# Kernel tuning notes

Hardware: AMD Instinct MI355X
Metric: run time of the kernel (lower is better)

## Reference

```python
import jax, jax.numpy as jnp
import numpy as np

GROUPS = 3
EPS = 1e-5

def _conv(x, w, groups, pad):
    # x: NCHW, w: OIHW (grouped). pad: 'VALID' for 1x1, ((1,1),(1,1)) for 3x3 same.
    return jax.lax.conv_general_dilated(
        x, w, window_strides=(1, 1), padding=pad,
        feature_group_count=groups,
        dimension_numbers=('NCHW', 'OIHW', 'NCHW'))

def _bn(x, g, b, m, v):
    # folded inference batchnorm: y = x*scale + (beta - mean*scale)
    s = g / jnp.sqrt(v + EPS)
    return x * s[None, :, None, None] + (b - m * s)[None, :, None, None]

def _shuffle(x, groups):
    B, C, H, W = x.shape
    return x.reshape(B, groups, C // groups, H, W).transpose(0, 2, 1, 3, 4).reshape(B, C, H, W)

def setup_inputs() -> dict:
    key = jax.random.key(0)
    ks = jax.random.split(key, 16)
    B, Cin, Cout, H, W = 64, 480, 480, 28, 28
    mid = Cout // 4  # 120
    d = {}
    d['x'] = jax.random.normal(ks[0], (B, Cin, H, W), jnp.float32)
    d['w1'] = jax.random.normal(ks[1], (mid, Cin // GROUPS, 1, 1), jnp.float32) * 0.05
    d['g1'] = jax.random.uniform(ks[2], (mid,), jnp.float32)
    d['b1'] = jax.random.normal(ks[3], (mid,), jnp.float32)
    d['m1'] = jax.random.normal(ks[4], (mid,), jnp.float32)
    d['v1'] = jax.random.uniform(ks[5], (mid,), jnp.float32)
    d['w2'] = jax.random.normal(ks[6], (mid, 1, 3, 3), jnp.float32) * 0.05
    d['g2'] = jax.random.uniform(ks[7], (mid,), jnp.float32)
    d['b2'] = jax.random.normal(ks[8], (mid,), jnp.float32)
    d['m2'] = jax.random.normal(ks[9], (mid,), jnp.float32)
    d['v2'] = jax.random.uniform(ks[10], (mid,), jnp.float32)
    d['w3'] = jax.random.normal(ks[11], (Cout, mid // GROUPS, 1, 1), jnp.float32) * 0.05
    d['g3'] = jax.random.uniform(ks[12], (Cout,), jnp.float32)
    d['b3'] = jax.random.normal(ks[13], (Cout,), jnp.float32)
    d['m3'] = jax.random.normal(ks[14], (Cout,), jnp.float32)
    d['v3'] = jax.random.uniform(ks[15], (Cout,), jnp.float32)
    return d

def reference(x, w1, g1, b1, m1, v1, w2, g2, b2, m2, v2, w3, g3, b3, m3, v3):
    mid = w2.shape[0]
    shortcut = x  # in_channels == out_channels -> identity shortcut
    out = jax.nn.relu(_bn(_conv(x, w1, GROUPS, 'VALID'), g1, b1, m1, v1))
    out = _bn(_conv(out, w2, mid, ((1, 1), (1, 1))), g2, b2, m2, v2)  # depthwise 3x3
    out = _shuffle(out, GROUPS)
    out = jax.nn.relu(_bn(_conv(out, w3, GROUPS, 'VALID'), g3, b3, m3, v3))
    return out + shortcut
```

## Files before the change

### kernel.cpp

```cpp
#include <hip/hip_runtime.h>


namespace {
constexpr int CIN = 480;
constexpr int MID = 120;
constexpr int HWP = 784;
constexpr float EPSV = 1e-5f;

constexpr size_t TMP1_N = (size_t)64 * MID * HWP;
constexpr int WA1_N = 3 * 3 * 5 * 64 * 8;
constexpr int WA3_N = 3 * 10 * 2 * 64 * 8;

constexpr int S1W = 84;
constexpr int S1O = 65;
constexpr int S2O = 69;
constexpr int S3O = 67;
}

typedef short bf16x8 __attribute__((ext_vector_type(8)));
typedef float f32x4  __attribute__((ext_vector_type(4)));

__device__ inline unsigned short f2bf(float v) {
    unsigned u = __float_as_uint(v);
    return (unsigned short)((u + 0x7fffu + ((u >> 16) & 1u)) >> 16);
}
__device__ inline float bf2f(unsigned s) {
    return __uint_as_float(s << 16);
}
__device__ inline void split2(float v, unsigned short& h, unsigned short& l) {
    h = f2bf(v);
    l = f2bf(v - bf2f((unsigned)h));
}

__global__ __launch_bounds__(256) void prep_k(
    const float* __restrict__ w1, const float* __restrict__ w3,
    const float* __restrict__ g1, const float* __restrict__ b1,
    const float* __restrict__ m1, const float* __restrict__ v1,
    const float* __restrict__ g2, const float* __restrict__ b2,
    const float* __restrict__ m2, const float* __restrict__ v2,
    const float* __restrict__ g3, const float* __restrict__ b3,
    const float* __restrict__ m3, const float* __restrict__ v3,
    float* __restrict__ par, unsigned short* __restrict__ wpk)
{
    const int t = blockIdx.x * 256 + threadIdx.x;
    if (t < 720) {
        if (t < 120) {
            const float s = g1[t] * rsqrtf(v1[t] + EPSV);
            par[t] = s; par[120 + t] = fmaf(-m1[t], s, b1[t]);
        } else if (t < 240) {
            const int c = t - 120;
            const float s = g2[c] * rsqrtf(v2[c] + EPSV);
            par[240 + c] = s; par[360 + c] = fmaf(-m2[c], s, b2[c]);
        } else {
            const int c = t - 240;
            const float s = g3[c] * rsqrtf(v3[c] + EPSV);
            par[480 + c] = s; par[960 + c] = fmaf(-m3[c], s, b3[c]);
        }
    } else if (t < 3600) {
        const int t1   = t - 720;
        const int lane = t1 & 63;
        const int rest = t1 >> 6;
        const int ks   = rest % 5;
        const int mtg  = rest / 5;
        const int mt   = mtg % 3;
        const int g    = mtg / 3;
        const int row  = mt * 16 + (lane & 15);
        const int k0   = ks * 32 + (lane >> 4) * 8;
        unsigned short h[8], l[8];
#pragma unroll
        for (int j = 0; j < 8; ++j) {
            float v = (row < 40) ? w1[(size_t)(g * 40 + row) * 160 + k0 + j] : 0.f;
            split2(v, h[j], l[j]);
        }
        *reinterpret_cast<uint4*>(wpk + (size_t)t1 * 8)         = *reinterpret_cast<uint4*>(h);
        *reinterpret_cast<uint4*>(wpk + WA1_N + (size_t)t1 * 8) = *reinterpret_cast<uint4*>(l);
    } else if (t < 7440) {
        const int t3   = t - 3600;
        const int lane = t3 & 63;
        const int rest = t3 >> 6;
        const int ks   = rest % 2;
        const int mtg  = rest / 2;
        const int mt   = mtg % 10;
        const int g    = mtg / 10;
        const int row  = mt * 16 + (lane & 15);
        const int k0   = ks * 32 + (lane >> 4) * 8;
        unsigned short h[8], l[8];
#pragma unroll
        for (int j = 0; j < 8; ++j) {
            const int k = k0 + j;
            float v = (k < 40) ? w3[(size_t)(g * 160 + row) * 40 + k] : 0.f;
            split2(v, h[j], l[j]);
        }
        *reinterpret_cast<uint4*>(wpk + 2 * WA1_N + (size_t)t3 * 8)         = *reinterpret_cast<uint4*>(h);
        *reinterpret_cast<uint4*>(wpk + 2 * WA1_N + WA3_N + (size_t)t3 * 8) = *reinterpret_cast<uint4*>(l);
    }
}

__global__ __launch_bounds__(256) void k1_mfma(
    const float* __restrict__ x, const unsigned short* __restrict__ wA1h,
    const float* __restrict__ par, unsigned short* __restrict__ tmp1)
{
    __shared__ __align__(16) unsigned xs32[64 * S1W];
    __shared__ float sL[40], shL[40];

    const int tid  = threadIdx.x;
    const int lane = tid & 63;
    const int wv   = tid >> 6;
    const int g    = blockIdx.y;
    const int p0   = blockIdx.x * 64;

    if (tid < 40) { sL[tid] = par[g * 40 + tid]; shL[tid] = par[120 + g * 40 + tid]; }

    const int px4s = (tid >> 4) & 15;
    {
        const int ps = p0 + px4s * 4;
        const int bs = ps / HWP;
        const int hws = ps - bs * HWP;
        const float* __restrict__ xb = x + ((size_t)bs * CIN + g * 160) * HWP + hws;

        float4 v0[5], v1[5];
#pragma unroll
        for (int i = 0; i < 5; ++i) {
            const int cp = (tid & 15) + 16 * i;
            v0[i] = *reinterpret_cast<const float4*>(xb + (size_t)(2 * cp)     * HWP);
            v1[i] = *reinterpret_cast<const float4*>(xb + (size_t)(2 * cp + 1) * HWP);
        }
#pragma unroll
        for (int i = 0; i < 5; ++i) {
            const int cp = (tid & 15) + 16 * i;
            unsigned* d = xs32 + (px4s * 4) * S1W + cp;
            d[0]       = (unsigned)f2bf(v0[i].x) | ((unsigned)f2bf(v1[i].x) << 16);
            d[S1W]     = (unsigned)f2bf(v0[i].y) | ((unsigned)f2bf(v1[i].y) << 16);
            d[2 * S1W] = (unsigned)f2bf(v0[i].z) | ((unsigned)f2bf(v1[i].z) << 16);
            d[3 * S1W] = (unsigned)f2bf(v0[i].w) | ((unsigned)f2bf(v1[i].w) << 16);
        }
    }
    __syncthreads();

    const unsigned short* __restrict__ wA1l = wA1h + WA1_N;
    const unsigned short* xsh = reinterpret_cast<const unsigned short*>(xs32);
    f32x4 acc[3];
#pragma unroll
    for (int mt = 0; mt < 3; ++mt) acc[mt] = f32x4{0.f, 0.f, 0.f, 0.f};

    const int n16 = lane & 15;
    const int kq  = lane >> 4;
    const int pxl = wv * 16 + n16;
#pragma unroll
    for (int ks = 0; ks < 5; ++ks) {
        const bf16x8 Bv = *reinterpret_cast<const bf16x8*>(
            xsh + pxl * (2 * S1W) + ks * 32 + kq * 8);
#pragma unroll
        for (int mt = 0; mt < 3; ++mt) {
            const size_t fi = (((size_t)(g * 3 + mt) * 5 + ks) * 64 + lane) * 8;
            const bf16x8 Ah = *reinterpret_cast<const bf16x8*>(wA1h + fi);
            const bf16x8 Al = *reinterpret_cast<const bf16x8*>(wA1l + fi);
            acc[mt] = __builtin_amdgcn_mfma_f32_16x16x32_bf16(Ah, Bv, acc[mt], 0, 0, 0);
            acc[mt] = __builtin_amdgcn_mfma_f32_16x16x32_bf16(Al, Bv, acc[mt], 0, 0, 0);
        }
    }
    __syncthreads();

    float* osr = reinterpret_cast<float*>(xs32);
    {
#pragma unroll
        for (int mt = 0; mt < 3; ++mt) {
#pragma unroll
            for (int r = 0; r < 4; ++r) {
                const int ocl = mt * 16 + kq * 4 + r;
                if (ocl < 40) {
                    float val = fmaf(acc[mt][r], sL[ocl], shL[ocl]);
                    osr[ocl * S1O + pxl] = val > 0.f ? val : 0.f;
                }
            }
        }
    }
    __syncthreads();

#pragma unroll
    for (int i = 0; i < 3; ++i) {
        const int task = tid + i * 256;
        if (task < 640) {
            const int ocl = task >> 4;
            const int px4 = task & 15;
            const int p   = p0 + px4 * 4;
            const int b   = p / HWP;
            const int hw  = p - b * HWP;
            const float* s = osr + ocl * S1O + px4 * 4;
            const unsigned lo = (unsigned)f2bf(s[0]) | ((unsigned)f2bf(s[1]) << 16);
            const unsigned hi = (unsigned)f2bf(s[2]) | ((unsigned)f2bf(s[3]) << 16);
            *reinterpret_cast<uint2*>(
                tmp1 + ((size_t)b * MID + g * 40 + ocl) * HWP + hw) = make_uint2(lo, hi);
        }
    }
}

__global__ __launch_bounds__(256) void k3_fused(
    const unsigned short* __restrict__ tmp1, const float* __restrict__ w2,
    const unsigned short* __restrict__ wA3h, const float* __restrict__ par,
    const float* __restrict__ x, float* __restrict__ out)
{
    __shared__ __align__(16) float uni[160 * S3O];
    __shared__ float sL[160], shL[160];

    float* dout = uni;
    unsigned short* Bfr = reinterpret_cast<unsigned short*>(uni + 40 * S2O);
    float* osr = uni;

    const int tid  = threadIdx.x;
    const int lane = tid & 63;
    const int wv   = tid >> 6;
    const int bx   = blockIdx.x;
    const int gk   = blockIdx.y;
    const int p0   = bx * 64;

    if (tid < 160) {
        sL[tid]  = par[480 + gk * 160 + tid];
        shL[tid] = par[960 + gk * 160 + tid];
    }
    if (tid < 192)
        *reinterpret_cast<uint4*>(Bfr + 2560 + tid * 8) = make_uint4(0u, 0u, 0u, 0u);

#pragma unroll
    for (int i = 0; i < 3; ++i) {
        const int task = tid + i * 256;
        if (task < 640) {
            const int csl = task >> 4;
            const int px4 = task & 15;
            const int cs  = gk * 40 + csl;
            const int c   = (cs % 3) * 40 + cs / 3;
            const int p   = p0 + px4 * 4;
            const int b   = p / HWP;
            const int hw  = p - b * HWP;
            const int h   = hw / 28, w = hw - h * 28;
            const unsigned short* __restrict__ in = tmp1 + ((size_t)b * MID + c) * HWP;
            const float* __restrict__ wk = w2 + c * 9;

            float a0 = 0.f, a1 = 0.f, a2 = 0.f, a3 = 0.f;
#pragma unroll
            for (int dh = -1; dh <= 1; ++dh) {
                const int hh = h + dh;
                if (hh < 0 || hh > 27) continue;
                const unsigned short* r = in + hh * 28 + w;
                const uint2 cc = *reinterpret_cast<const uint2*>(r);
                const float c0 = bf2f(cc.x & 0xffffu), c1 = bf2f(cc.x >> 16);
                const float c2 = bf2f(cc.y & 0xffffu), c3 = bf2f(cc.y >> 16);
                const float cl = (w > 0)  ? bf2f(r[-1]) : 0.f;
                const float cr = (w < 24) ? bf2f(r[4])  : 0.f;
                const float* wr = wk + (dh + 1) * 3;
                a0 = fmaf(cl, wr[0], a0); a0 = fmaf(c0, wr[1], a0); a0 = fmaf(c1, wr[2], a0);
                a1 = fmaf(c0, wr[0], a1); a1 = fmaf(c1, wr[1], a1); a1 = fmaf(c2, wr[2], a1);
                a2 = fmaf(c1, wr[0], a2); a2 = fmaf(c2, wr[1], a2); a2 = fmaf(c3, wr[2], a2);
                a3 = fmaf(c2, wr[0], a3); a3 = fmaf(c3, wr[1], a3); a3 = fmaf(cr, wr[2], a3);
            }
            const float s  = par[240 + c];
            const float sh = par[360 + c];
            float* d = dout + csl * S2O + px4 * 4;
            d[0] = fmaf(a0, s, sh); d[1] = fmaf(a1, s, sh);
            d[2] = fmaf(a2, s, sh); d[3] = fmaf(a3, s, sh);
        }
    }
    __syncthreads();

    {
        const int task = tid;
#pragma unroll
        for (int i = 0; i < 2; ++i) {
            const int t2 = task + i * 256;
            if (t2 < 320) {
                const int cb  = t2 >> 6;
                const int pxl = t2 & 63;
                unsigned short res[8];
#pragma unroll
                for (int j = 0; j < 8; ++j)
                    res[j] = f2bf(dout[(cb * 8 + j) * S2O + pxl]);
                const int ks = cb >> 2, kbl = cb & 3;
                const int nt = pxl >> 4, n16 = pxl & 15;
                *reinterpret_cast<uint4*>(
                    Bfr + (((ks * 4 + kbl) * 4 + nt) * 16 + n16) * 8) =
                    *reinterpret_cast<uint4*>(res);
            }
        }
    }
    __syncthreads();

    const unsigned short* __restrict__ wA3l = wA3h + WA3_N;
    f32x4 acc[10];
#pragma unroll
    for (int mt = 0; mt < 10; ++mt) acc[mt] = f32x4{0.f, 0.f, 0.f, 0.f};

    const int kbl = lane >> 4, n16 = lane & 15;
    const int nt  = wv;
#pragma unroll
    for (int ks = 0; ks < 2; ++ks) {
        const bf16x8 Bv = *reinterpret_cast<const bf16x8*>(
            Bfr + (((ks * 4 + kbl) * 4 + nt) * 16 + n16) * 8);
#pragma unroll
        for (int mt = 0; mt < 10; ++mt) {
            const size_t fi = (((size_t)(gk * 10 + mt) * 2 + ks) * 64 + lane) * 8;
            const bf16x8 Ah = *reinterpret_cast<const bf16x8*>(wA3h + fi);
            const bf16x8 Al = *reinterpret_cast<const bf16x8*>(wA3l + fi);
            acc[mt] = __builtin_amdgcn_mfma_f32_16x16x32_bf16(Ah, Bv, acc[mt], 0, 0, 0);
            acc[mt] = __builtin_amdgcn_mfma_f32_16x16x32_bf16(Al, Bv, acc[mt], 0, 0, 0);
        }
    }
    __syncthreads();

    {
        const int kq = lane >> 4;
        const int pxl = nt * 16 + n16;
#pragma unroll
        for (int mt = 0; mt < 10; ++mt) {
#pragma unroll
            for (int r = 0; r < 4; ++r) {
                const int ocl = mt * 16 + kq * 4 + r;
                float val = fmaf(acc[mt][r], sL[ocl], shL[ocl]);
                osr[ocl * S3O + pxl] = val > 0.f ? val : 0.f;
            }
        }
    }
    __syncthreads();

#pragma unroll
    for (int i = 0; i < 10; ++i) {
        const int task = tid + i * 256;
        const int ocl  = task >> 4;
        const int px4  = task & 15;
        const int p    = p0 + px4 * 4;
        const int b    = p / HWP;
        const int hw   = p - b * HWP;
        const int oc   = gk * 160 + ocl;
        const size_t idx = ((size_t)b * CIN + oc) * HWP + hw;
        const float* s = osr + ocl * S3O + px4 * 4;
        const float4 sc = *reinterpret_cast<const float4*>(x + idx);
        float4 o;
        o.x = s[0] + sc.x; o.y = s[1] + sc.y;
        o.z = s[2] + sc.z; o.w = s[3] + sc.w;
        *reinterpret_cast<float4*>(out + idx) = o;
    }
}

extern "C" void kernel_launch(void* const* d_in, const int* in_sizes, int n_in,
                              void* d_out, int out_size, void* d_ws, size_t ws_size,
                              hipStream_t stream) {
    const float* x  = (const float*)d_in[0];
    const float* w1 = (const float*)d_in[1];
    const float* g1 = (const float*)d_in[2];
    const float* b1 = (const float*)d_in[3];
    const float* m1 = (const float*)d_in[4];
    const float* v1 = (const float*)d_in[5];
    const float* w2 = (const float*)d_in[6];
    const float* g2 = (const float*)d_in[7];
    const float* b2 = (const float*)d_in[8];
    const float* m2 = (const float*)d_in[9];
    const float* v2 = (const float*)d_in[10];
    const float* w3 = (const float*)d_in[11];
    const float* g3 = (const float*)d_in[12];
    const float* b3 = (const float*)d_in[13];
    const float* m3 = (const float*)d_in[14];
    const float* v3 = (const float*)d_in[15];
    float* out = (float*)d_out;

    float* wsf = (float*)d_ws;
    unsigned short* tmp1 = (unsigned short*)wsf;
    float* par = wsf + TMP1_N / 2;
    unsigned short* wpk = (unsigned short*)(par + 1440);

    prep_k<<<30, 256, 0, stream>>>(w1, w3, g1, b1, m1, v1, g2, b2, m2, v2,
                                   g3, b3, m3, v3, par, wpk);
    k1_mfma<<<dim3(784, 3), 256, 0, stream>>>(x, wpk, par, tmp1);
    k3_fused<<<dim3(784, 3), 256, 0, stream>>>(tmp1, w2, wpk + 2 * WA1_N, par, x, out);
}
```

Measured before the change: 105.4 us.

## Split depthwise conv into separate kernel and write conv3 output directly from registers

Pulls the depthwise 3x3 conv out of the fused conv3 kernel into its own kernel that processes all 120 channels per pixel tile, writing a shuffled bf16 intermediate (tmp2). The conv3 MFMA kernel now reads the pre-shuffled tmp2, builds its B fragments, prefetches the residual x into registers before the MFMA loop, and writes outputs directly without the LDS staging and two extra barriers. The aim is to stop recomputing the depthwise conv three times (once per output group) and to cut LDS traffic and syncs. In exchange it adds a kernel launch, a full extra bf16 intermediate round trip through global memory, and uncoalesced scalar global stores and x loads in the epilogue.

```diff
diff --git a/kernel.cpp b/kernel.cpp
--- a/kernel.cpp
+++ b/kernel.cpp
@@ -14,7 +14,6 @@
 constexpr int S1W = 84;
 constexpr int S1O = 65;
 constexpr int S2O = 69;
-constexpr int S3O = 67;
 }
 
 typedef short bf16x8 __attribute__((ext_vector_type(8)));
@@ -195,46 +194,34 @@
     }
 }
 
-__global__ __launch_bounds__(256) void k3_fused(
+__global__ __launch_bounds__(256) void k2_dw(
     const unsigned short* __restrict__ tmp1, const float* __restrict__ w2,
-    const unsigned short* __restrict__ wA3h, const float* __restrict__ par,
-    const float* __restrict__ x, float* __restrict__ out)
+    const float* __restrict__ par, unsigned short* __restrict__ tmp2)
 {
-    __shared__ __align__(16) float uni[160 * S3O];
-    __shared__ float sL[160], shL[160];
-
-    float* dout = uni;
-    unsigned short* Bfr = reinterpret_cast<unsigned short*>(uni + 40 * S2O);
-    float* osr = uni;
-
-    const int tid  = threadIdx.x;
-    const int lane = tid & 63;
-    const int wv   = tid >> 6;
-    const int bx   = blockIdx.x;
-    const int gk   = blockIdx.y;
-    const int p0   = bx * 64;
-
-    if (tid < 160) {
-        sL[tid]  = par[480 + gk * 160 + tid];
-        shL[tid] = par[960 + gk * 160 + tid];
-    }
-    if (tid < 192)
-        *reinterpret_cast<uint4*>(Bfr + 2560 + tid * 8) = make_uint4(0u, 0u, 0u, 0u);
-
-#pragma unroll
-    for (int i = 0; i < 3; ++i) {
+    __shared__ float dout[MID * S2O];
+    __shared__ float w2s[1080];
+    __shared__ float s2s[120], sh2s[120];
+
+    const int tid = threadIdx.x;
+    const int bx  = blockIdx.x;
+    const int p0  = bx * 64;
+
+    for (int i = tid; i < 1080; i += 256) w2s[i] = w2[i];
+    if (tid < 120) { s2s[tid] = par[240 + tid]; sh2s[tid] = par[360 + tid]; }
+    __syncthreads();
+
+#pragma unroll
+    for (int i = 0; i < 8; ++i) {
         const int task = tid + i * 256;
-        if (task < 640) {
-            const int csl = task >> 4;
+        if (task < 1920) {
+            const int ch  = task >> 4;
             const int px4 = task & 15;
-            const int cs  = gk * 40 + csl;
-            const int c   = (cs % 3) * 40 + cs / 3;
             const int p   = p0 + px4 * 4;
             const int b   = p / HWP;
             const int hw  = p - b * HWP;
             const int h   = hw / 28, w = hw - h * 28;
-            const unsigned short* __restrict__ in = tmp1 + ((size_t)b * MID + c) * HWP;
-            const float* __restrict__ wk = w2 + c * 9;
+            const unsigned short* __restrict__ in = tmp1 + ((size_t)b * MID + ch) * HWP;
+            const float* wk = w2s + ch * 9;
 
             float a0 = 0.f, a1 = 0.f, a2 = 0.f, a3 = 0.f;
 #pragma unroll
@@ -253,33 +240,97 @@
                 a2 = fmaf(c1, wr[0], a2); a2 = fmaf(c2, wr[1], a2); a2 = fmaf(c3, wr[2], a2);
                 a3 = fmaf(c2, wr[0], a3); a3 = fmaf(c3, wr[1], a3); a3 = fmaf(cr, wr[2], a3);
             }
-            const float s  = par[240 + c];
-            const float sh = par[360 + c];
-            float* d = dout + csl * S2O + px4 * 4;
+            const float s  = s2s[ch];
+            const float sh = sh2s[ch];
+            const int gi = ch / 40;
+            const int cs = (ch - gi * 40) * 3 + gi;
+            float* d = dout + cs * S2O + px4 * 4;
             d[0] = fmaf(a0, s, sh); d[1] = fmaf(a1, s, sh);
             d[2] = fmaf(a2, s, sh); d[3] = fmaf(a3, s, sh);
         }
     }
     __syncthreads();
 
-    {
-        const int task = tid;
-#pragma unroll
-        for (int i = 0; i < 2; ++i) {
-            const int t2 = task + i * 256;
-            if (t2 < 320) {
-                const int cb  = t2 >> 6;
-                const int pxl = t2 & 63;
-                unsigned short res[8];
-#pragma unroll
-                for (int j = 0; j < 8; ++j)
-                    res[j] = f2bf(dout[(cb * 8 + j) * S2O + pxl]);
-                const int ks = cb >> 2, kbl = cb & 3;
-                const int nt = pxl >> 4, n16 = pxl & 15;
-                *reinterpret_cast<uint4*>(
-                    Bfr + (((ks * 4 + kbl) * 4 + nt) * 16 + n16) * 8) =
-                    *reinterpret_cast<uint4*>(res);
+#pragma unroll
+    for (int i = 0; i < 4; ++i) {
+        const int task = tid + i * 256;
+        if (task < 960) {
+            const int cs  = task >> 3;
+            const int px8 = task & 7;
+            const int p   = p0 + px8 * 8;
+            const int b   = p / HWP;
+            const int hw  = p - b * HWP;
+            const float* dr = dout + cs * S2O + px8 * 8;
+            uint4 o;
+            o.x = (unsigned)f2bf(dr[0]) | ((unsigned)f2bf(dr[1]) << 16);
+            o.y = (unsigned)f2bf(dr[2]) | ((unsigned)f2bf(dr[3]) << 16);
+            o.z = (unsigned)f2bf(dr[4]) | ((unsigned)f2bf(dr[5]) << 16);
+            o.w = (unsigned)f2bf(dr[6]) | ((unsigned)f2bf(dr[7]) << 16);
+            *reinterpret_cast<uint4*>(
+                tmp2 + ((size_t)b * MID + cs) * HWP + hw) = o;
+        }
+    }
+}
+
+__global__ __launch_bounds__(256) void k3_mfma(
+    const unsigned short* __restrict__ tmp2, const unsigned short* __restrict__ wA3h,
+    const float* __restrict__ par,
+    const float* __restrict__ x, float* __restrict__ out)
+{
+    __shared__ __align__(16) unsigned short Bfr[4096];
+    __shared__ float sL[160], shL[160];
+
+    const int tid  = threadIdx.x;
+    const int lane = tid & 63;
+    const int wv   = tid >> 6;
+    const int bx   = blockIdx.x;
+    const int gk   = blockIdx.y;
+    const int p0   = bx * 64;
+
+    if (tid < 160) {
+        sL[tid]  = par[480 + gk * 160 + tid];
+        shL[tid] = par[960 + gk * 160 + tid];
+    }
+    if (tid < 192)
+        *reinterpret_cast<uint4*>(Bfr + 2560 + tid * 8) = make_uint4(0u, 0u, 0u, 0u);
+
+#pragma unroll
+    for (int i = 0; i < 3; ++i) {
+        const int task = tid + i * 256;
+        if (task < 640) {
+            const int csl = task >> 4;
+            const int px4 = task & 15;
+            const int p   = p0 + px4 * 4;
+            const int b   = p / HWP;
+            const int hw  = p - b * HWP;
+            const uint2 cc = *reinterpret_cast<const uint2*>(
+                tmp2 + ((size_t)b * MID + gk * 40 + csl) * HWP + hw);
+            const int kb8 = csl >> 3, j = csl & 7;
+            unsigned short vals[4] = {
+                (unsigned short)(cc.x & 0xffffu), (unsigned short)(cc.x >> 16),
+                (unsigned short)(cc.y & 0xffffu), (unsigned short)(cc.y >> 16) };
+#pragma unroll
+            for (int pp = 0; pp < 4; ++pp) {
+                const int px  = px4 * 4 + pp;
+                const int nt  = px >> 4, n16 = px & 15;
+                Bfr[((kb8 * 4 + nt) * 16 + n16) * 8 + j] = vals[pp];
             }
+        }
+    }
+
+    const int n16 = lane & 15, kq = lane >> 4;
+    const int pxl = wv * 16 + n16;
+    const int pg  = p0 + pxl;
+    const int bg  = pg / HWP;
+    const int hwg = pg - bg * HWP;
+    const size_t xbase = (size_t)bg * CIN * HWP + hwg;
+    float xv[10][4];
+#pragma unroll
+    for (int mt = 0; mt < 10; ++mt) {
+#pragma unroll
+        for (int r = 0; r < 4; ++r) {
+            const int oc = gk * 160 + mt * 16 + kq * 4 + r;
+            xv[mt][r] = x[xbase + (size_t)oc * HWP];
         }
     }
     __syncthreads();
@@ -289,12 +340,11 @@
 #pragma unroll
     for (int mt = 0; mt < 10; ++mt) acc[mt] = f32x4{0.f, 0.f, 0.f, 0.f};
 
-    const int kbl = lane >> 4, n16 = lane & 15;
-    const int nt  = wv;
 #pragma unroll
     for (int ks = 0; ks < 2; ++ks) {
+        const int kb8 = ks * 4 + kq;
         const bf16x8 Bv = *reinterpret_cast<const bf16x8*>(
-            Bfr + (((ks * 4 + kbl) * 4 + nt) * 16 + n16) * 8);
+            Bfr + ((kb8 * 4 + wv) * 16 + n16) * 8);
 #pragma unroll
         for (int mt = 0; mt < 10; ++mt) {
             const size_t fi = (((size_t)(gk * 10 + mt) * 2 + ks) * 64 + lane) * 8;
@@ -304,39 +354,17 @@
             acc[mt] = __builtin_amdgcn_mfma_f32_16x16x32_bf16(Al, Bv, acc[mt], 0, 0, 0);
         }
     }
-    __syncthreads();
-
-    {
-        const int kq = lane >> 4;
-        const int pxl = nt * 16 + n16;
-#pragma unroll
-        for (int mt = 0; mt < 10; ++mt) {
-#pragma unroll
-            for (int r = 0; r < 4; ++r) {
-                const int ocl = mt * 16 + kq * 4 + r;
-                float val = fmaf(acc[mt][r], sL[ocl], shL[ocl]);
-                osr[ocl * S3O + pxl] = val > 0.f ? val : 0.f;
-            }
-        }
-    }
-    __syncthreads();
-
-#pragma unroll
-    for (int i = 0; i < 10; ++i) {
-        const int task = tid + i * 256;
-        const int ocl  = task >> 4;
-        const int px4  = task & 15;
-        const int p    = p0 + px4 * 4;
-        const int b    = p / HWP;
-        const int hw   = p - b * HWP;
-        const int oc   = gk * 160 + ocl;
-        const size_t idx = ((size_t)b * CIN + oc) * HWP + hw;
-        const float* s = osr + ocl * S3O + px4 * 4;
-        const float4 sc = *reinterpret_cast<const float4*>(x + idx);
-        float4 o;
-        o.x = s[0] + sc.x; o.y = s[1] + sc.y;
-        o.z = s[2] + sc.z; o.w = s[3] + sc.w;
-        *reinterpret_cast<float4*>(out + idx) = o;
+
+#pragma unroll
+    for (int mt = 0; mt < 10; ++mt) {
+#pragma unroll
+        for (int r = 0; r < 4; ++r) {
+            const int ocl = mt * 16 + kq * 4 + r;
+            const int oc  = gk * 160 + ocl;
+            float val = fmaf(acc[mt][r], sL[ocl], shL[ocl]);
+            val = val > 0.f ? val : 0.f;
+            out[xbase + (size_t)oc * HWP] = val + xv[mt][r];
+        }
     }
 }
 
@@ -361,13 +389,14 @@
     const float* v3 = (const float*)d_in[15];
     float* out = (float*)d_out;
 
-    float* wsf = (float*)d_ws;
-    unsigned short* tmp1 = (unsigned short*)wsf;
-    float* par = wsf + TMP1_N / 2;
+    unsigned short* tmp1 = (unsigned short*)d_ws;
+    unsigned short* tmp2 = tmp1 + TMP1_N;
+    float* par = (float*)(tmp2 + TMP1_N);
     unsigned short* wpk = (unsigned short*)(par + 1440);
 
     prep_k<<<30, 256, 0, stream>>>(w1, w3, g1, b1, m1, v1, g2, b2, m2, v2,
                                    g3, b3, m3, v3, par, wpk);
     k1_mfma<<<dim3(784, 3), 256, 0, stream>>>(x, wpk, par, tmp1);
-    k3_fused<<<dim3(784, 3), 256, 0, stream>>>(tmp1, w2, wpk + 2 * WA1_N, par, x, out);
-}
+    k2_dw  <<<784,          256, 0, stream>>>(tmp1, w2, par, tmp2);
+    k3_mfma<<<dim3(784, 3), 256, 0, stream>>>(tmp2, wpk + 2 * WA1_N, par, x, out);
+}
```

Result: slower. 118.0 us (+12.0%).
